# Performance work log

Measured on AMD Instinct MI355X. Metric: run time of the kernel, lower is better.

The kernel has to match this reference:

```python
import jax, jax.numpy as jnp
import numpy as np

P = 8        # patch_size
S = 4        # stride
NV = 31      # nvals
DELTA = 0.05
ETA = 0.01
TAU = 0.1
H = W = 256
C = 3
HP = (H - P) // S + 1
WP = (W - P) // S + 1

_lin = jnp.linspace(-1.0, 1.0, P)
# torch.meshgrid 'ij': meshy varies along rows, meshx along cols; shape (1,P,P,1,1)
YG = jnp.broadcast_to(_lin[:, None], (P, P))[None, :, :, None, None]
XG = jnp.broadcast_to(_lin[None, :], (P, P))[None, :, :, None, None]


def unfold(x):
    # x: (b,c,H,W) -> (b,c,P,P,hp,wp)
    i = (jnp.arange(HP) * S)[:, None] + jnp.arange(P)[None, :]  # (hp,P)
    j = (jnp.arange(WP) * S)[:, None] + jnp.arange(P)[None, :]  # (wp,P)
    pat = x[:, :, i[:, None, :, None], j[None, :, None, :]]    # (b,c,hp,wp,P,P)
    return jnp.transpose(pat, (0, 1, 4, 5, 2, 3))


def fold(patches):
    # patches: (b,c,P,P,hp,wp) -> (b,c,H,W) via overlap-add
    b, c = patches.shape[:2]
    i = (jnp.arange(HP) * S)[:, None] + jnp.arange(P)[None, :]  # (hp,P)
    j = (jnp.arange(WP) * S)[:, None] + jnp.arange(P)[None, :]
    ii = jnp.broadcast_to(i.T[:, None, :, None], (P, P, HP, WP))
    jj = jnp.broadcast_to(j.T[None, :, None, :], (P, P, HP, WP))
    out = jnp.zeros((b, c, H, W), patches.dtype)
    return out.at[:, :, ii, jj].add(patches)


def params_to_distances(params):
    # params: (N,5,hp,wp) -> distances (N,2,P,P,hp,wp)
    x0 = params[:, 3][:, None, None]  # (N,1,1,hp,wp)
    y0 = params[:, 4][:, None, None]
    angles = jnp.sort(jnp.remainder(params[:, :3], 2 * jnp.pi), axis=1)
    a1 = angles[:, 0][:, None, None]
    a2 = angles[:, 1][:, None, None]
    a3 = angles[:, 2][:, None, None]
    a4 = 0.5 * (a1 + a3) + jnp.where(
        jnp.remainder(0.5 * (a1 - a3), 2 * jnp.pi) >= jnp.pi, jnp.pi, 0.0)

    def g(dt):
        return (dt / jnp.pi - 1.0) ** 35

    def hline(a):
        return -jnp.sin(a) * (XG - x0) + jnp.cos(a) * (YG - y0)

    r42 = jnp.remainder(a2 - a4, 2 * jnp.pi)
    sgn42 = jnp.where(r42 < jnp.pi, 1.0, -1.0)
    d42 = sgn42 * jnp.minimum(sgn42 * hline(a4), -sgn42 * hline(a2)) + g(r42) * TAU

    r13 = jnp.remainder(a3 - a1, 2 * jnp.pi)
    sgn13 = jnp.where(r13 < jnp.pi, 1.0, -1.0)
    d13 = sgn13 * jnp.minimum(sgn13 * hline(a1), -sgn13 * hline(a3)) + g(r13) * TAU
    return jnp.stack([d13, d42], axis=1)


def distances_to_indicators(dists):
    # dists: (N,2,P,P,hp,wp) -> wedges (N,3,P,P,hp,wp)
    h = 0.5 * (1.0 + (2.0 / jnp.pi) * jnp.arctan(dists / ETA))
    return jnp.stack([1.0 - h[:, 0], h[:, 0] * (1.0 - h[:, 1]), h[:, 0] * h[:, 1]], axis=1)


def distances_to_boundaries(dists):
    d1 = dists[:, 0:1]
    d2 = dists[:, 1:2]
    minabs = jnp.where(d1 < 0.0, -d1,
                       jnp.where(d2 < 0.0, jnp.minimum(d1, -d2), jnp.minimum(d1, d2)))
    return 1.0 / (1.0 + (minabs / DELTA) ** 2)


def colors_and_patches(wedges, img_pat):
    # wedges: (N,3,P,P,hp,wp); img_pat: (1,c,P,P,hp,wp)
    num = jnp.einsum('cijhw,nkijhw->nckhw', img_pat[0], wedges)
    den = wedges.sum(axis=(2, 3))  # (N,3,hp,wp)
    colors = num / (den[:, None] + 1e-10)  # (N,c,3,hp,wp)
    patches = jnp.einsum('nkijhw,nckhw->ncijhw', wedges, colors)
    return colors, patches


def setup_inputs() -> dict:
    key = jax.random.key(0)
    x = jax.random.uniform(key, (1, C, H, W), dtype=jnp.float32)
    return {"x": x}


def reference(x):
    img_pat = unfold(x)  # (1,c,P,P,hp,wp)
    num_patches = fold(jnp.ones((1, 1, P, P, HP, WP), x.dtype))[0, 0]  # (H,W)

    angle_range = jnp.linspace(0.0, 2 * np.pi, NV + 1)[:NV]
    xy_range = jnp.linspace(-3.0, 3.0, NV)

    params = jnp.zeros((1, 5, HP, WP), x.dtype)
    # Coordinate-descent grid search over the 5 junction parameters
    for i in range(5):
        rng = angle_range if i < 3 else xy_range
        pq = jnp.tile(params, (NV, 1, 1, 1))
        pq = pq.at[:, i].add(rng[:, None, None])
        dists = params_to_distances(pq)
        wedges = distances_to_indicators(dists)
        _, patches = colors_and_patches(wedges, img_pat)
        loss = ((img_pat - patches) ** 2).mean(axis=(1, 2, 3))  # (NV,hp,wp)
        best = jnp.argmin(loss, axis=0)                          # (hp,wp)
        params = params.at[0, i].set(params[0, i] + rng[best])

    dists = params_to_distances(params)
    wedges = distances_to_indicators(dists)
    _, patches = colors_and_patches(wedges, img_pat)
    global_image = fold(patches) / num_patches
    local_boundaries = distances_to_boundaries(dists)  # (1,1,P,P,hp,wp)
    global_boundaries = fold(local_boundaries) / num_patches
    return global_image, global_boundaries
```

## Files before the change

### kernel.cpp

```cpp
#include <hip/hip_runtime.h>
#include <math.h>

#define WP_ 63
#define NPATCH 3969
#define PI_D 3.141592653589793
#define TWO_PI_D 6.283185307179586476925287
#define BANDF 4e-3f

typedef float f32x2 __attribute__((ext_vector_type(2)));
__device__ __forceinline__ f32x2 v2(float s) { return (f32x2){s, s}; }
__device__ __forceinline__ f32x2 fma2(f32x2 a, f32x2 b, f32x2 c) {
  return __builtin_elementwise_fma(a, b, c);
}

__device__ __forceinline__ double remtp_d(double v) {
  double r = (v < 0.0) ? v + TWO_PI_D : v;
  r = (r < 0.0) ? r + TWO_PI_D : r;
  r = (r >= TWO_PI_D) ? r - TWO_PI_D : r;
  return r;
}

__device__ __forceinline__ double lin8d(int i) {
  if (i == 7) return 1.0;
  return __dadd_rn(__dmul_rn((double)i, 2.0 / 7.0), -1.0);
}
__device__ __forceinline__ double angd(int n) {
  return __dmul_rn((double)n, TWO_PI_D / 31.0);
}
__device__ __forceinline__ double xyd(int n) {
  if (n == 30) return 3.0;
  return __dadd_rn(__dmul_rn((double)n, 6.0 / 30.0), -3.0);
}

__device__ __forceinline__ double pow35_d(double x) {
#pragma clang fp contract(off)
  double x2 = x * x;
  double r = x * x2;
  double b = x2 * x2;
  b = b * b; b = b * b; b = b * b;
  return r * b;
}

__device__ __forceinline__ double rcp_nr(double d) {
  double r;
  asm("v_rcp_f64 %0, %1" : "=v"(r) : "v"(d));
  r = fma(fma(-d, r, 1.0), r, r);
  r = fma(fma(-d, r, 1.0), r, r);
  return r;
}

__device__ __forceinline__ void sincos_fast(double x, double* so, double* co) {
  double kd = rint(x * 6.36619772367581382433e-01);
  int q = (int)kd & 3;
  double r = fma(-kd, 1.57079632673412561417e+00, x);
  r = fma(-kd, 6.07710050650619224932e-11, r);
  double z = r * r;
  double ps = 1.58969099521155010221e-10;
  ps = fma(z, ps, -2.50507602534068634195e-08);
  ps = fma(z, ps, 2.75573137070700676789e-06);
  ps = fma(z, ps, -1.98412698298579493134e-04);
  ps = fma(z, ps, 8.33333333332248946124e-03);
  ps = fma(z, ps, -1.66666666666666324348e-01);
  double sr = fma(z * r, ps, r);
  double pc = -1.13596475577881948265e-11;
  pc = fma(z, pc, 2.08757232129817482790e-09);
  pc = fma(z, pc, -2.75573143513906633035e-07);
  pc = fma(z, pc, 2.48015872894767294178e-05);
  pc = fma(z, pc, -1.38888888888741095749e-03);
  pc = fma(z, pc, 4.16666666666666019037e-02);
  double cr = fma(z, fma(z, pc, -0.5), 1.0);
  bool swp = q & 1;
  double s0 = swp ? cr : sr;
  double c0 = swp ? sr : cr;
  *so = (q & 2) ? -s0 : s0;
  *co = (((q + 1) & 2)) ? -c0 : c0;
}

#define TABN 57
__device__ __forceinline__ void build_atan_tab(double2* tab, float2* tabf) {
  int k = threadIdx.x;
  if (k < 56) {
    int hi = ((4076 + k) << 18) | (1 << 17);
    double c = __hiloint2double(hi, 0);
    double a = atan(c);
    tab[k] = double2{c, a};
    tabf[k + 1] = float2{(float)c, (float)a};
  } else if (k == 56) {
    tab[56] = double2{0.0, 0.0};
    tabf[0] = float2{0.0f, 0.0f};
  }
}

__device__ __forceinline__ void hstep2_tab(const double2* __restrict__ tab,
                                           double da, double db,
                                           double& ha, double& hb) {
  double za = da * 100.0, zb = db * 100.0;
  double ua = fabs(za), ub = fabs(zb);
  int ia = (__double2hiint(ua) >> 18) - 4076;
  int ib = (__double2hiint(ub) >> 18) - 4076;
  ia = (ia < 0) ? 56 : ((ia > 55) ? 55 : ia);
  ib = (ib < 0) ? 56 : ((ib > 55) ? 55 : ib);
  double2 ea = tab[ia];
  double2 eb = tab[ib];
  double ta = (ua - ea.x) * rcp_nr(fma(ua, ea.x, 1.0));
  double tb = (ub - eb.x) * rcp_nr(fma(ub, eb.x, 1.0));
  double z2a = ta * ta, z2b = tb * tb;
  double pa = 1.0 / 13.0, pb = 1.0 / 13.0;
  pa = fma(z2a, pa, -1.0 / 11.0); pb = fma(z2b, pb, -1.0 / 11.0);
  pa = fma(z2a, pa, 1.0 / 9.0);   pb = fma(z2b, pb, 1.0 / 9.0);
  pa = fma(z2a, pa, -1.0 / 7.0);  pb = fma(z2b, pb, -1.0 / 7.0);
  pa = fma(z2a, pa, 1.0 / 5.0);   pb = fma(z2b, pb, 1.0 / 5.0);
  pa = fma(z2a, pa, -1.0 / 3.0);  pb = fma(z2b, pb, -1.0 / 3.0);
  pa = fma(z2a, pa, 1.0);         pb = fma(z2b, pb, 1.0);
  double aa = fma(ta, pa, ea.y);
  double ab = fma(tb, pb, eb.y);
  aa = copysign(aa, za);
  ab = copysign(ab, zb);
  ha = fma(aa, 0.31830988618379067154, 0.5);
  hb = fma(ab, 0.31830988618379067154, 0.5);
}

__device__ __forceinline__ f32x2 hstepv(const float2* __restrict__ tabf,
                                        f32x2 d) {
  f32x2 z = d * 100.0f;
  f32x2 u = __builtin_elementwise_abs(z);
  int ia = (int)(__float_as_uint(u.x) >> 21) - 492;
  int ib = (int)(__float_as_uint(u.y) >> 21) - 492;
  ia = min(max(ia, -1), 55) + 1;
  ib = min(max(ib, -1), 55) + 1;
  float2 ea = tabf[ia], eb = tabf[ib];
  f32x2 ec = {ea.x, eb.x};
  f32x2 ey = {ea.y, eb.y};
  f32x2 den = fma2(u, ec, v2(1.0f));
  float ra, rb;
  asm("v_rcp_f32 %0, %1" : "=v"(ra) : "v"(den.x));
  asm("v_rcp_f32 %0, %1" : "=v"(rb) : "v"(den.y));
  f32x2 r = {ra, rb};
  f32x2 t = (u - ec) * r;
  f32x2 p = fma2(t * t, v2(-0.33333334f), v2(1.0f));
  f32x2 a = fma2(t, p, ey);
  a = __builtin_elementwise_copysign(a, z);
  return fma2(a, v2(0.31830987f), v2(0.5f));
}

struct JPd {
  double s1, c1, s2, c2, s3, c3, s4, c4;
  double sg13, sg42, gt13, gt42;
};

__device__ JPd jprep_d(double p0, double p1, double p2) {
#pragma clang fp contract(off)
  double r0 = remtp_d(p0), r1 = remtp_d(p1), r2 = remtp_d(p2);
  double mn = fmin(r0, r1), mx = fmax(r0, r1);
  double a1 = fmin(mn, r2);
  double a3 = fmax(mx, r2);
  double a2 = fmax(mn, fmin(mx, r2));
  double remm = remtp_d(0.5 * (a1 - a3));
  double a4 = 0.5 * (a1 + a3) + ((remm >= PI_D) ? PI_D : 0.0);
  JPd j;
  double r42 = remtp_d(a2 - a4);
  j.sg42 = (r42 < PI_D) ? 1.0 : -1.0;
  j.gt42 = pow35_d(r42 / PI_D - 1.0) * 0.1;
  double r13 = remtp_d(a3 - a1);
  j.sg13 = (r13 < PI_D) ? 1.0 : -1.0;
  j.gt13 = pow35_d(r13 / PI_D - 1.0) * 0.1;
  sincos_fast(a1, &j.s1, &j.c1);
  sincos_fast(a2, &j.s2, &j.c2);
  sincos_fast(a3, &j.s3, &j.c3);
  sincos_fast(a4, &j.s4, &j.c4);
  return j;
}

__device__ __forceinline__ void jdist_d(const JPd& j, double dx, double dy,
                                        double& d13, double& d42) {
  double hl1 = (-j.s1) * dx + j.c1 * dy;
  double hl2 = (-j.s2) * dx + j.c2 * dy;
  double hl3 = (-j.s3) * dx + j.c3 * dy;
  double hl4 = (-j.s4) * dx + j.c4 * dy;
  d13 = j.sg13 * fmin(j.sg13 * hl1, (-j.sg13) * hl3) + j.gt13;
  d42 = j.sg42 * fmin(j.sg42 * hl4, (-j.sg42) * hl2) + j.gt42;
}

__global__ void __launch_bounds__(256)
foj_descent(const float* __restrict__ x, double* __restrict__ pout) {
  const int tid = threadIdx.x;
  const int wv = tid >> 6;
  const int lane = tid & 63;
  const int hp = lane >> 5;
  const int cand = lane & 31;
  const int patch = blockIdx.x * 4 + wv;

  __shared__ double2 stab[TABN];
  __shared__ float2 stabf[TABN + 1];
  __shared__ float4 simg[4][64];
  __shared__ float simgp[4][3][64];
  build_atan_tab(stab, stabf);
  if (patch < NPATCH) {
    int ph = patch / WP_;
    int pw = patch - ph * WP_;
    int py = lane >> 3, pxx = lane & 7;
    int base = (ph * 4 + py) * 256 + (pw * 4 + pxx);
    float4 v;
    v.x = x[base];
    v.y = x[65536 + base];
    v.z = x[131072 + base];
    v.w = 0.0f;
    simg[wv][lane] = v;
    simgp[wv][0][lane] = v.x;
    simgp[wv][1][lane] = v.y;
    simgp[wv][2][lane] = v.z;
  }
  __syncthreads();
  if (patch >= NPATCH) return;
  const float4* sp = simg[wv];

  double sx0 = 0.0, sx1 = 0.0, sx2 = 0.0;
  {
    const float4* hbase = sp + hp * 32;
#pragma unroll
    for (int t = 0; t < 32; ++t) {
      float4 im = hbase[t];
      sx0 += (double)im.x; sx1 += (double)im.y; sx2 += (double)im.z;
    }
    sx0 += __shfl_xor(sx0, 32);
    sx1 += __shfl_xor(sx1, 32);
    sx2 += __shfl_xor(sx2, 32);
  }
  const float sx0f = (float)sx0, sx1f = (float)sx1, sx2f = (float)sx2;

  const double vlinx = lin8d(lane & 7);
  const double vliny = lin8d(lane >> 3);
  const float4 vim = sp[lane];

  double q0 = 0.0, q1 = 0.0, q2 = 0.0, q3 = 0.0, q4 = 0.0;

#pragma unroll 1
  for (int i = 0; i < 5; ++i) {
    double rv = (i < 3) ? angd(cand) : xyd(cand);
    double p0 = q0 + ((i == 0) ? rv : 0.0);
    double p1 = q1 + ((i == 1) ? rv : 0.0);
    double p2 = q2 + ((i == 2) ? rv : 0.0);
    double x0 = q3 + ((i == 3) ? rv : 0.0);
    double y0 = q4 + ((i == 4) ? rv : 0.0);

    JPd j = jprep_d(p0, p1, p2);

    float blf;
    {
      f32x2 ns1v = v2((float)(-j.s1)), ns2v = v2((float)(-j.s2));
      f32x2 ns3v = v2((float)(-j.s3)), ns4v = v2((float)(-j.s4));
      float c1f = (float)j.c1, c2f = (float)j.c2;
      float c3f = (float)j.c3, c4f = (float)j.c4;
      f32x2 sg13v = v2((float)j.sg13), sg42v = v2((float)j.sg42);
      f32x2 nsg13v = -sg13v, nsg42v = -sg42v;
      f32x2 gt13v = v2((float)j.gt13), gt42v = v2((float)j.gt42);
      f32x2 dxp[4];
#pragma unroll
      for (int t = 0; t < 4; ++t)
        dxp[t] = (f32x2){(float)(lin8d(2 * t) - x0),
                         (float)(lin8d(2 * t + 1) - x0)};

      f32x2 den0v = {0, 0}, den1v = {0, 0}, den2v = {0, 0};
      f32x2 n00v = {0, 0}, n01v = {0, 0}, n10v = {0, 0}, n11v = {0, 0};
      f32x2 n20v = {0, 0}, n21v = {0, 0};
      f32x2 W00v = {0, 0}, W01v = {0, 0}, W11v = {0, 0};
#pragma unroll 1
      for (int r = 0; r < 4; ++r) {
        int iyy = hp * 4 + r;
        double liny = (iyy == 7) ? 1.0
                    : __dadd_rn(__dmul_rn((double)iyy, 2.0 / 7.0), -1.0);
        float dyf = (float)(liny - y0);
        f32x2 cdy1 = v2(c1f * dyf), cdy2 = v2(c2f * dyf);
        f32x2 cdy3 = v2(c3f * dyf), cdy4 = v2(c4f * dyf);
        const float* q0p = &simgp[wv][0][hp * 32 + r * 8];
        const float* q1p = &simgp[wv][1][hp * 32 + r * 8];
        const float* q2p = &simgp[wv][2][hp * 32 + r * 8];
#pragma unroll
        for (int cp = 0; cp < 4; ++cp) {
          f32x2 dxv = dxp[cp];
          f32x2 hl1 = fma2(ns1v, dxv, cdy1);
          f32x2 hl3 = fma2(ns3v, dxv, cdy3);
          f32x2 hl4 = fma2(ns4v, dxv, cdy4);
          f32x2 hl2 = fma2(ns2v, dxv, cdy2);
          f32x2 d13 = fma2(sg13v,
              __builtin_elementwise_min(sg13v * hl1, nsg13v * hl3), gt13v);
          f32x2 d42 = fma2(sg42v,
              __builtin_elementwise_min(sg42v * hl4, nsg42v * hl2), gt42v);
          f32x2 h1 = hstepv(stabf, d13);
          f32x2 h2 = hstepv(stabf, d42);
          f32x2 w0 = v2(1.0f) - h1;
          f32x2 om = v2(1.0f) - h2;
          f32x2 w1 = h1 * om;
          f32x2 w2 = h1 * h2;
          f32x2 i0 = *(const f32x2*)(q0p + 2 * cp);
          f32x2 i1 = *(const f32x2*)(q1p + 2 * cp);
          f32x2 i2 = *(const f32x2*)(q2p + 2 * cp);
          den0v += w0; den1v += w1; den2v += w2;
          n00v = fma2(i0, w0, n00v); n01v = fma2(i0, w1, n01v);
          n10v = fma2(i1, w0, n10v); n11v = fma2(i1, w1, n11v);
          n20v = fma2(i2, w0, n20v); n21v = fma2(i2, w1, n21v);
          W00v = fma2(w0, w0, W00v); W01v = fma2(w0, w1, W01v);
          W11v = fma2(w1, w1, W11v);
        }
      }
      float den0f = den0v.x + den0v.y, den1f = den1v.x + den1v.y;
      float den2f = den2v.x + den2v.y;
      float n00f = n00v.x + n00v.y, n01f = n01v.x + n01v.y;
      float n10f = n10v.x + n10v.y, n11f = n11v.x + n11v.y;
      float n20f = n20v.x + n20v.y, n21f = n21v.x + n21v.y;
      float W00f = W00v.x + W00v.y, W01f = W01v.x + W01v.y;
      float W11f = W11v.x + W11v.y;

      den0f += __shfl_xor(den0f, 32); den1f += __shfl_xor(den1f, 32); den2f += __shfl_xor(den2f, 32);
      n00f += __shfl_xor(n00f, 32); n01f += __shfl_xor(n01f, 32);
      n10f += __shfl_xor(n10f, 32); n11f += __shfl_xor(n11f, 32);
      n20f += __shfl_xor(n20f, 32); n21f += __shfl_xor(n21f, 32);
      W00f += __shfl_xor(W00f, 32); W01f += __shfl_xor(W01f, 32); W11f += __shfl_xor(W11f, 32);

      float n02f = sx0f - n00f - n01f;
      float n12f = sx1f - n10f - n11f;
      float n22f = sx2f - n20f - n21f;
      float W02f = den0f - W00f - W01f;
      float W12f = den1f - W01f - W11f;
      float W22f = den2f - W02f - W12f;

      float e0 = den0f + 1e-10f, e1 = den1f + 1e-10f, e2 = den2f + 1e-10f;
      float r0f, r1f, r2f;
      asm("v_rcp_f32 %0, %1" : "=v"(r0f) : "v"(e0));
      asm("v_rcp_f32 %0, %1" : "=v"(r1f) : "v"(e1));
      asm("v_rcp_f32 %0, %1" : "=v"(r2f) : "v"(e2));
      r0f = fmaf(fmaf(-e0, r0f, 1.0f), r0f, r0f);
      r1f = fmaf(fmaf(-e1, r1f, 1.0f), r1f, r1f);
      r2f = fmaf(fmaf(-e2, r2f, 1.0f), r2f, r2f);
      float c00 = n00f * r0f, c01 = n01f * r1f, c02 = n02f * r2f;
      float c10 = n10f * r0f, c11 = n11f * r1f, c12 = n12f * r2f;
      float c20 = n20f * r0f, c21 = n21f * r1f, c22 = n22f * r2f;

      float lossf =
          c00 * (W00f * c00 + W01f * c01 + W02f * c02 - 2.0f * n00f) +
          c01 * (W01f * c00 + W11f * c01 + W12f * c02 - 2.0f * n01f) +
          c02 * (W02f * c00 + W12f * c01 + W22f * c02 - 2.0f * n02f) +
          c10 * (W00f * c10 + W01f * c11 + W02f * c12 - 2.0f * n10f) +
          c11 * (W01f * c10 + W11f * c11 + W12f * c12 - 2.0f * n11f) +
          c12 * (W02f * c10 + W12f * c11 + W22f * c12 - 2.0f * n12f) +
          c20 * (W00f * c20 + W01f * c21 + W02f * c22 - 2.0f * n20f) +
          c21 * (W01f * c20 + W11f * c21 + W12f * c22 - 2.0f * n21f) +
          c22 * (W02f * c20 + W12f * c21 + W22f * c22 - 2.0f * n22f);

      blf = (cand < 31) ? lossf : 3.0e38f;
    }

    float mnf = blf;
#pragma unroll
    for (int m = 1; m <= 16; m <<= 1) mnf = fminf(mnf, __shfl_xor(mnf, m));
    bool inb = (cand < 31) && (blf <= mnf + BANDF);
    unsigned bal32 = (unsigned)__ballot(inb);

    int bi;
    if (__popc(bal32) == 1) {
      bi = __ffs(bal32) - 1;
    } else {
      double bestLoss = (double)INFINITY;
      int bi0 = 0;
      unsigned rem = bal32;
#pragma unroll 1
      while (rem) {
        int c = __ffs(rem) - 1;
        rem &= rem - 1;
        double rvc = (i < 3) ? angd(c) : xyd(c);
        double x0c = q3 + ((i == 3) ? rvc : 0.0);
        double y0c = q4 + ((i == 4) ? rvc : 0.0);
        JPd jc;
        jc.s1 = __shfl(j.s1, c);  jc.c1 = __shfl(j.c1, c);
        jc.s2 = __shfl(j.s2, c);  jc.c2 = __shfl(j.c2, c);
        jc.s3 = __shfl(j.s3, c);  jc.c3 = __shfl(j.c3, c);
        jc.s4 = __shfl(j.s4, c);  jc.c4 = __shfl(j.c4, c);
        jc.sg13 = __shfl(j.sg13, c); jc.sg42 = __shfl(j.sg42, c);
        jc.gt13 = __shfl(j.gt13, c); jc.gt42 = __shfl(j.gt42, c);

        double d13, d42;
        jdist_d(jc, vlinx - x0c, vliny - y0c, d13, d42);
        double h1, h2;
        hstep2_tab(stab, d13, d42, h1, h2);
        double w0 = 1.0 - h1;
        double w1 = h1 * (1.0 - h2);
        double w2 = h1 * h2;
        double ix = (double)vim.x, iy2 = (double)vim.y, iz = (double)vim.z;
        double s0 = w0, s1 = w1, s2 = w2;
        double s3 = ix * w0, s4 = ix * w1;
        double s5 = iy2 * w0, s6 = iy2 * w1;
        double s7 = iz * w0, s8 = iz * w1;
        double s9 = w0 * w0, s10 = w0 * w1, s11 = w1 * w1;
#pragma unroll
        for (int m = 1; m <= 32; m <<= 1) {
          s0 += __shfl_xor(s0, m);  s1 += __shfl_xor(s1, m);
          s2 += __shfl_xor(s2, m);  s3 += __shfl_xor(s3, m);
          s4 += __shfl_xor(s4, m);  s5 += __shfl_xor(s5, m);
          s6 += __shfl_xor(s6, m);  s7 += __shfl_xor(s7, m);
          s8 += __shfl_xor(s8, m);  s9 += __shfl_xor(s9, m);
          s10 += __shfl_xor(s10, m); s11 += __shfl_xor(s11, m);
        }
        double den0 = s0, den1 = s1, den2 = s2;
        double n00 = s3, n01 = s4, n10 = s5, n11 = s6, n20 = s7, n21 = s8;
        double W00 = s9, W01 = s10, W11 = s11;

        double n02 = sx0 - n00 - n01;
        double n12 = sx1 - n10 - n11;
        double n22 = sx2 - n20 - n21;
        double W02 = den0 - W00 - W01;
        double W12 = den1 - W01 - W11;
        double W22 = den2 - W02 - W12;

        double r0 = rcp_nr(den0 + 1e-10);
        double r1 = rcp_nr(den1 + 1e-10);
        double r2 = rcp_nr(den2 + 1e-10);
        double c00 = n00 * r0, c01 = n01 * r1, c02 = n02 * r2;
        double c10 = n10 * r0, c11 = n11 * r1, c12 = n12 * r2;
        double c20 = n20 * r0, c21 = n21 * r1, c22 = n22 * r2;

        double loss =
            c00 * (W00 * c00 + W01 * c01 + W02 * c02 - 2.0 * n00) +
            c01 * (W01 * c00 + W11 * c01 + W12 * c02 - 2.0 * n01) +
            c02 * (W02 * c00 + W12 * c01 + W22 * c02 - 2.0 * n02) +
            c10 * (W00 * c10 + W01 * c11 + W02 * c12 - 2.0 * n10) +
            c11 * (W01 * c10 + W11 * c11 + W12 * c12 - 2.0 * n11) +
            c12 * (W02 * c10 + W12 * c11 + W22 * c12 - 2.0 * n12) +
            c20 * (W00 * c20 + W01 * c21 + W02 * c22 - 2.0 * n20) +
            c21 * (W01 * c20 + W11 * c21 + W12 * c22 - 2.0 * n21) +
            c22 * (W02 * c20 + W12 * c21 + W22 * c22 - 2.0 * n22);

        if (loss < bestLoss) { bestLoss = loss; bi0 = c; }
      }
      bi = bi0;
    }

    double upd = (i < 3) ? angd(bi) : xyd(bi);
    if (i == 0) q0 += upd;
    else if (i == 1) q1 += upd;
    else if (i == 2) q2 += upd;
    else if (i == 3) q3 += upd;
    else q4 += upd;
  }

  if (lane == 0) {
    pout[patch * 5 + 0] = q0;
    pout[patch * 5 + 1] = q1;
    pout[patch * 5 + 2] = q2;
    pout[patch * 5 + 3] = q3;
    pout[patch * 5 + 4] = q4;
  }
}

__global__ void __launch_bounds__(256) foj_final(const float* __restrict__ x,
                                                 const double* __restrict__ pin,
                                                 float* __restrict__ out) {
  int lane = threadIdx.x & 63;
  int patch = blockIdx.x * 4 + (threadIdx.x >> 6);
  if (patch >= NPATCH) return;
  int ph = patch / WP_;
  int pw = patch - ph * WP_;
  double q0 = pin[patch * 5 + 0];
  double q1 = pin[patch * 5 + 1];
  double q2 = pin[patch * 5 + 2];
  double x0 = pin[patch * 5 + 3];
  double y0 = pin[patch * 5 + 4];

  JPd j = jprep_d(q0, q1, q2);
  int pi2 = lane >> 3, pj = lane & 7;
  double dx = lin8d(pj) - x0;
  double dy = lin8d(pi2) - y0;
  double d13, d42;
  jdist_d(j, dx, dy, d13, d42);
  double h1 = 0.5 + 0.31830988618379067154 * atan(d13 * 100.0);
  double h2 = 0.5 + 0.31830988618379067154 * atan(d42 * 100.0);
  double w0 = 1.0 - h1;
  double w1 = h1 * (1.0 - h2);
  double w2 = h1 * h2;

  int oy = ph * 4 + pi2, ox = pw * 4 + pj;
  double im0 = (double)x[oy * 256 + ox];
  double im1 = (double)x[65536 + oy * 256 + ox];
  double im2 = (double)x[131072 + oy * 256 + ox];

  double red[12] = {w0, w1, w2,
                    im0 * w0, im0 * w1, im0 * w2,
                    im1 * w0, im1 * w1, im1 * w2,
                    im2 * w0, im2 * w1, im2 * w2};
#pragma unroll
  for (int t = 0; t < 12; ++t) {
    double v = red[t];
#pragma unroll
    for (int m = 1; m <= 32; m <<= 1) v += __shfl_xor(v, m);
    red[t] = v;
  }
  double e0 = red[0] + 1e-10, e1 = red[1] + 1e-10, e2 = red[2] + 1e-10;
  double pv0 = w0 * (red[3] / e0) + w1 * (red[4] / e1) + w2 * (red[5] / e2);
  double pv1 = w0 * (red[6] / e0) + w1 * (red[7] / e1) + w2 * (red[8] / e2);
  double pv2 = w0 * (red[9] / e0) + w1 * (red[10] / e1) + w2 * (red[11] / e2);

  double minabs = (d13 < 0.0) ? -d13
                              : ((d42 < 0.0) ? fmin(d13, -d42) : fmin(d13, d42));
  double tb = minabs / 0.05;
  double bnd = 1.0 / (1.0 + tb * tb);

  atomicAdd(&out[oy * 256 + ox], (float)pv0);
  atomicAdd(&out[65536 + oy * 256 + ox], (float)pv1);
  atomicAdd(&out[131072 + oy * 256 + ox], (float)pv2);
  atomicAdd(&out[196608 + oy * 256 + ox], (float)bnd);
}

__global__ void __launch_bounds__(256) foj_norm(float* __restrict__ out) {
  int idx = blockIdx.x * 256 + threadIdx.x;
  int y = idx >> 8, xx = idx & 255;
  int hlo = (y >= 4) ? ((y - 4) >> 2) : 0;
  int hhi = min(62, y >> 2);
  int wlo = (xx >= 4) ? ((xx - 4) >> 2) : 0;
  int whi = min(62, xx >> 2);
  float np_ = (float)((hhi - hlo + 1) * (whi - wlo + 1));
  out[idx] /= np_;
  out[65536 + idx] /= np_;
  out[131072 + idx] /= np_;
  out[196608 + idx] /= np_;
}

extern "C" void kernel_launch(void* const* d_in, const int* in_sizes, int n_in,
                              void* d_out, int out_size, void* d_ws, size_t ws_size,
                              hipStream_t stream) {
  const float* x = (const float*)d_in[0];
  float* out = (float*)d_out;
  double* pws = (double*)d_ws;

  foj_descent<<<(NPATCH + 3) / 4, 256, 0, stream>>>(x, pws);
  hipMemsetAsync(d_out, 0, (size_t)out_size * sizeof(float), stream);
  foj_final<<<(NPATCH + 3) / 4, 256, 0, stream>>>(x, pws, out);
  foj_norm<<<256, 256, 0, stream>>>(out);
}
```

Before: 101.5 us.

## Use one-wave blocks per patch and derive third wedge weight sum algebraically

The descent kernel now launches one 64-thread block per patch instead of packing four patches into each 256-thread block. The block-wide barrier then only waits on one wave, and the patch bounds check goes away. The third wedge's denominator is now computed as 64 minus the other two weight sums, since the three weights sum to one per pixel. This drops one accumulator and one shuffle reduction in both the float and double loss paths. The cost is that the atan table is rebuilt four times as often, once per block, and there are many more small blocks, which may limit occupancy through the per-CU block count.

```diff
diff --git a/kernel.cpp b/kernel.cpp
--- a/kernel.cpp
+++ b/kernel.cpp
@@ -181,21 +181,19 @@
   d42 = j.sg42 * fmin(j.sg42 * hl4, (-j.sg42) * hl2) + j.gt42;
 }
 
-__global__ void __launch_bounds__(256)
+__global__ void __launch_bounds__(64)
 foj_descent(const float* __restrict__ x, double* __restrict__ pout) {
-  const int tid = threadIdx.x;
-  const int wv = tid >> 6;
-  const int lane = tid & 63;
+  const int lane = threadIdx.x;
   const int hp = lane >> 5;
   const int cand = lane & 31;
-  const int patch = blockIdx.x * 4 + wv;
+  const int patch = blockIdx.x;
 
   __shared__ double2 stab[TABN];
   __shared__ float2 stabf[TABN + 1];
-  __shared__ float4 simg[4][64];
-  __shared__ float simgp[4][3][64];
+  __shared__ float4 simg[64];
+  __shared__ float simgp[3][64];
   build_atan_tab(stab, stabf);
-  if (patch < NPATCH) {
+  {
     int ph = patch / WP_;
     int pw = patch - ph * WP_;
     int py = lane >> 3, pxx = lane & 7;
@@ -205,14 +203,13 @@
     v.y = x[65536 + base];
     v.z = x[131072 + base];
     v.w = 0.0f;
-    simg[wv][lane] = v;
-    simgp[wv][0][lane] = v.x;
-    simgp[wv][1][lane] = v.y;
-    simgp[wv][2][lane] = v.z;
+    simg[lane] = v;
+    simgp[0][lane] = v.x;
+    simgp[1][lane] = v.y;
+    simgp[2][lane] = v.z;
   }
   __syncthreads();
-  if (patch >= NPATCH) return;
-  const float4* sp = simg[wv];
+  const float4* sp = simg;
 
   double sx0 = 0.0, sx1 = 0.0, sx2 = 0.0;
   {
@@ -260,7 +257,7 @@
         dxp[t] = (f32x2){(float)(lin8d(2 * t) - x0),
                          (float)(lin8d(2 * t + 1) - x0)};
 
-      f32x2 den0v = {0, 0}, den1v = {0, 0}, den2v = {0, 0};
+      f32x2 den0v = {0, 0}, den1v = {0, 0};
       f32x2 n00v = {0, 0}, n01v = {0, 0}, n10v = {0, 0}, n11v = {0, 0};
       f32x2 n20v = {0, 0}, n21v = {0, 0};
       f32x2 W00v = {0, 0}, W01v = {0, 0}, W11v = {0, 0};
@@ -272,9 +269,9 @@
         float dyf = (float)(liny - y0);
         f32x2 cdy1 = v2(c1f * dyf), cdy2 = v2(c2f * dyf);
         f32x2 cdy3 = v2(c3f * dyf), cdy4 = v2(c4f * dyf);
-        const float* q0p = &simgp[wv][0][hp * 32 + r * 8];
-        const float* q1p = &simgp[wv][1][hp * 32 + r * 8];
-        const float* q2p = &simgp[wv][2][hp * 32 + r * 8];
+        const float* q0p = &simgp[0][hp * 32 + r * 8];
+        const float* q1p = &simgp[1][hp * 32 + r * 8];
+        const float* q2p = &simgp[2][hp * 32 + r * 8];
 #pragma unroll
         for (int cp = 0; cp < 4; ++cp) {
           f32x2 dxv = dxp[cp];
@@ -291,11 +288,10 @@
           f32x2 w0 = v2(1.0f) - h1;
           f32x2 om = v2(1.0f) - h2;
           f32x2 w1 = h1 * om;
-          f32x2 w2 = h1 * h2;
           f32x2 i0 = *(const f32x2*)(q0p + 2 * cp);
           f32x2 i1 = *(const f32x2*)(q1p + 2 * cp);
           f32x2 i2 = *(const f32x2*)(q2p + 2 * cp);
-          den0v += w0; den1v += w1; den2v += w2;
+          den0v += w0; den1v += w1;
           n00v = fma2(i0, w0, n00v); n01v = fma2(i0, w1, n01v);
           n10v = fma2(i1, w0, n10v); n11v = fma2(i1, w1, n11v);
           n20v = fma2(i2, w0, n20v); n21v = fma2(i2, w1, n21v);
@@ -304,19 +300,19 @@
         }
       }
       float den0f = den0v.x + den0v.y, den1f = den1v.x + den1v.y;
-      float den2f = den2v.x + den2v.y;
       float n00f = n00v.x + n00v.y, n01f = n01v.x + n01v.y;
       float n10f = n10v.x + n10v.y, n11f = n11v.x + n11v.y;
       float n20f = n20v.x + n20v.y, n21f = n21v.x + n21v.y;
       float W00f = W00v.x + W00v.y, W01f = W01v.x + W01v.y;
       float W11f = W11v.x + W11v.y;
 
-      den0f += __shfl_xor(den0f, 32); den1f += __shfl_xor(den1f, 32); den2f += __shfl_xor(den2f, 32);
+      den0f += __shfl_xor(den0f, 32); den1f += __shfl_xor(den1f, 32);
       n00f += __shfl_xor(n00f, 32); n01f += __shfl_xor(n01f, 32);
       n10f += __shfl_xor(n10f, 32); n11f += __shfl_xor(n11f, 32);
       n20f += __shfl_xor(n20f, 32); n21f += __shfl_xor(n21f, 32);
       W00f += __shfl_xor(W00f, 32); W01f += __shfl_xor(W01f, 32); W11f += __shfl_xor(W11f, 32);
 
+      float den2f = 64.0f - den0f - den1f;
       float n02f = sx0f - n00f - n01f;
       float n12f = sx1f - n10f - n11f;
       float n22f = sx2f - n20f - n21f;
@@ -384,9 +380,8 @@
         hstep2_tab(stab, d13, d42, h1, h2);
         double w0 = 1.0 - h1;
         double w1 = h1 * (1.0 - h2);
-        double w2 = h1 * h2;
         double ix = (double)vim.x, iy2 = (double)vim.y, iz = (double)vim.z;
-        double s0 = w0, s1 = w1, s2 = w2;
+        double s0 = w0, s1 = w1;
         double s3 = ix * w0, s4 = ix * w1;
         double s5 = iy2 * w0, s6 = iy2 * w1;
         double s7 = iz * w0, s8 = iz * w1;
@@ -394,13 +389,14 @@
 #pragma unroll
         for (int m = 1; m <= 32; m <<= 1) {
           s0 += __shfl_xor(s0, m);  s1 += __shfl_xor(s1, m);
-          s2 += __shfl_xor(s2, m);  s3 += __shfl_xor(s3, m);
-          s4 += __shfl_xor(s4, m);  s5 += __shfl_xor(s5, m);
-          s6 += __shfl_xor(s6, m);  s7 += __shfl_xor(s7, m);
-          s8 += __shfl_xor(s8, m);  s9 += __shfl_xor(s9, m);
-          s10 += __shfl_xor(s10, m); s11 += __shfl_xor(s11, m);
+          s3 += __shfl_xor(s3, m);  s4 += __shfl_xor(s4, m);
+          s5 += __shfl_xor(s5, m);  s6 += __shfl_xor(s6, m);
+          s7 += __shfl_xor(s7, m);  s8 += __shfl_xor(s8, m);
+          s9 += __shfl_xor(s9, m);  s10 += __shfl_xor(s10, m);
+          s11 += __shfl_xor(s11, m);
         }
-        double den0 = s0, den1 = s1, den2 = s2;
+        double den0 = s0, den1 = s1;
+        double den2 = 64.0 - den0 - den1;
         double n00 = s3, n01 = s4, n10 = s5, n11 = s6, n20 = s7, n21 = s8;
         double W00 = s9, W01 = s10, W11 = s11;
 
@@ -530,7 +526,7 @@
   float* out = (float*)d_out;
   double* pws = (double*)d_ws;
 
-  foj_descent<<<(NPATCH + 3) / 4, 256, 0, stream>>>(x, pws);
+  foj_descent<<<NPATCH, 64, 0, stream>>>(x, pws);
   hipMemsetAsync(d_out, 0, (size_t)out_size * sizeof(float), stream);
   foj_final<<<(NPATCH + 3) / 4, 256, 0, stream>>>(x, pws, out);
   foj_norm<<<256, 256, 0, stream>>>(out);
```

Measured after the change: 100.5 us. No clear change (-1.0%).
